# Kernel tuning notes

Hardware: AMD Instinct MI355X
Metric: run time of the kernel (lower is better)

The kernel has to match this reference:

```python
import jax, jax.numpy as jnp
import numpy as np

FORGET_BIAS = 1.0  # TF LSTMCell default

def _lstm_step(c, h, x, W, b):
    # TF BasicLSTM/LSTMCell gate order: i, j (cell candidate), f, o
    z = jnp.concatenate([x, h], axis=-1) @ W + b
    i, j, f, o = jnp.split(z, 4, axis=-1)
    c_new = c * jax.nn.sigmoid(f + FORGET_BIAS) + jax.nn.sigmoid(i) * jnp.tanh(j)
    h_new = jnp.tanh(c_new) * jax.nn.sigmoid(o)
    return c_new, h_new

def setup_inputs() -> dict:
    key = jax.random.key(0)
    k1, k2, k3 = jax.random.split(key, 3)
    B, T, D, H1, H2 = 512, 2048, 1, 64, 1
    x = jax.random.normal(k1, (B, T, D), dtype=jnp.float32)
    W1 = jax.random.normal(k2, (D + H1, 4 * H1), dtype=jnp.float32) * 0.1
    b1 = jnp.zeros((4 * H1,), dtype=jnp.float32)
    W2 = jax.random.normal(k3, (H1 + H2, 4 * H2), dtype=jnp.float32) * 0.1
    b2 = jnp.zeros((4 * H2,), dtype=jnp.float32)
    return {"x": x, "W1": W1, "b1": b1, "W2": W2, "b2": b2}

def reference(x, W1, b1, W2, b2):
    B = x.shape[0]
    H1 = W1.shape[1] // 4
    H2 = W2.shape[1] // 4
    init = (jnp.zeros((B, H1), x.dtype), jnp.zeros((B, H1), x.dtype),
            jnp.zeros((B, H2), x.dtype), jnp.zeros((B, H2), x.dtype))

    def step(carry, x_t):
        c1, h1, c2, h2 = carry
        c1, h1 = _lstm_step(c1, h1, x_t, W1, b1)   # layer 1: LSTMCell(64)
        c2, h2 = _lstm_step(c2, h2, h1, W2, b2)    # layer 2: LSTMCell(1)
        return (c1, h1, c2, h2), h2

    xs = jnp.swapaxes(x, 0, 1)           # [T, B, 1]
    _, ys = jax.lax.scan(step, init, xs)  # ys: [T, B, 1]
    return jnp.swapaxes(ys, 0, 1)         # [B, T, 1]
```

## Files before the change

kernel.cpp:

```cpp
#include <hip/hip_runtime.h>

#define TT 2048
#define NB 256

typedef float v2f __attribute__((ext_vector_type(2)));

__device__ __forceinline__ v2f mk2(float a, float b) { v2f r; r.x = a; r.y = b; return r; }
__device__ __forceinline__ float rcpf(float x) { return __builtin_amdgcn_rcpf(x); }
__device__ __forceinline__ float fsig(float x) { return rcpf(1.0f + __expf(-x)); }
__device__ __forceinline__ float ftanh(float x) {
    return fmaf(2.0f, rcpf(1.0f + __expf(-2.0f * x)), -1.0f);
}

template<int C>
__device__ __forceinline__ float dppmov(float s) {
    return __int_as_float(__builtin_amdgcn_update_dpp(
        __float_as_int(s), __float_as_int(s), C, 0xF, 0xF, false));
}
template<int Q>
__device__ __forceinline__ float qbcast(float x) {
    return __int_as_float(__builtin_amdgcn_update_dpp(
        __float_as_int(x), __float_as_int(x), Q * 0x55, 0xF, 0xF, false));
}

__global__ __launch_bounds__(512)
__attribute__((amdgpu_waves_per_eu(2, 2)))
void lstm1_kernel(const float* __restrict__ x,
                  const float* __restrict__ W1,
                  const float* __restrict__ b1,
                  const float* __restrict__ W2,
                  float* __restrict__ zout)
{
    __shared__ __align__(16) float xall[2][TT + 4];
    __shared__ __align__(16) float h1row[2][64];
    __shared__ __align__(16) float part[2][2][4][4][72];
    __shared__ __align__(16) float zpart[2][32][4][4];

    const int tid  = threadIdx.x;
    const int wave = tid >> 6;
    const int lane = tid & 63;
    const int b    = blockIdx.x;

    for (int i = tid; i < TT; i += 512) {
        xall[0][i] = x[(2 * b) * TT + i];
        xall[1][i] = x[(2 * b + 1) * TT + i];
    }
    if (tid < 8) xall[tid & 1][TT + (tid >> 1)] = 0.0f;

    const int eid = wave >> 2;
    const int wq  = wave & 3;

#define DECLP(G, coff, p) const v2f w##G##p = \
    mk2(W1[(1 + 16*wq + 2*(p)) * 256 + (coff) + lane], \
        W1[(2 + 16*wq + 2*(p)) * 256 + (coff) + lane]);
    DECLP(I,   0, 0) DECLP(I,   0, 1) DECLP(I,   0, 2) DECLP(I,   0, 3)
    DECLP(I,   0, 4) DECLP(I,   0, 5) DECLP(I,   0, 6) DECLP(I,   0, 7)
    DECLP(J,  64, 0) DECLP(J,  64, 1) DECLP(J,  64, 2) DECLP(J,  64, 3)
    DECLP(J,  64, 4) DECLP(J,  64, 5) DECLP(J,  64, 6) DECLP(J,  64, 7)
    DECLP(F, 128, 0) DECLP(F, 128, 1) DECLP(F, 128, 2) DECLP(F, 128, 3)
    DECLP(F, 128, 4) DECLP(F, 128, 5) DECLP(F, 128, 6) DECLP(F, 128, 7)
    DECLP(O, 192, 0) DECLP(O, 192, 1) DECLP(O, 192, 2) DECLP(O, 192, 3)
    DECLP(O, 192, 4) DECLP(O, 192, 5) DECLP(O, 192, 6) DECLP(O, 192, 7)
#undef DECLP

    const int gB   = lane & 3;
    const int uB   = (wq << 4) + (lane >> 2);
    const int colB = (gB << 6) + uB;
    const float w0x   = W1[colB];
    const float biasF = b1[colB] + ((gB == 2) ? 1.0f : 0.0f);
    const float nlm   = (gB == 1) ? -2.0f : -1.0f;
    const bool  isj   = (gB == 1);
    const float w2own = W2[uB * 4 + gB];
    const int   gidx  = (12 + (lane & 3) + ((lane >> 2) << 4)) & 63;

    float c1 = 0.0f;

    if (tid < 128) ((float*)h1row)[tid] = 0.0f;
    __syncthreads();

    float* __restrict__ zb = zout + (size_t)(2 * b + eid) * TT * 4;

    float* __restrict__ pw = &part[eid][0][wq][0][lane];
    const float* __restrict__ pr = &part[eid][0][0][gB][uB];

#define PK4(p, hx, hy)                                                        \
    aI = __builtin_elementwise_fma(mk2(hx, hy), wI##p, aI);                   \
    aJ = __builtin_elementwise_fma(mk2(hx, hy), wJ##p, aJ);                   \
    aF = __builtin_elementwise_fma(mk2(hx, hy), wF##p, aF);                   \
    aO = __builtin_elementwise_fma(mk2(hx, hy), wO##p, aO);

#define STEP(P, t, xv)                                                        \
    {                                                                         \
              \
        if ((t) < TT) {                                                       \
            const float4* hp = (const float4*)&h1row[eid][wq << 4];           \
            const float4 q0 = hp[0], q1 = hp[1], q2 = hp[2], q3 = hp[3];      \
            v2f aI = mk2(0.f, 0.f), aJ = mk2(0.f, 0.f);                       \
            v2f aF = mk2(0.f, 0.f), aO = mk2(0.f, 0.f);                       \
            PK4(0, q0.x, q0.y) PK4(1, q0.z, q0.w)                             \
            PK4(2, q1.x, q1.y) PK4(3, q1.z, q1.w)                             \
            PK4(4, q2.x, q2.y) PK4(5, q2.z, q2.w)                             \
            PK4(6, q3.x, q3.y) PK4(7, q3.z, q3.w)                             \
            pw[(P)*1152 + 0*72] = aI.x + aI.y;                                \
            pw[(P)*1152 + 1*72] = aJ.x + aJ.y;                                \
            pw[(P)*1152 + 2*72] = aF.x + aF.y;                                \
            pw[(P)*1152 + 3*72] = aO.x + aO.y;                                \
        }                                                                     \
        __syncthreads();                       \
          \
        if ((t) >= 16 && (t) <= TT && ((t) & 15) == 0 &&                      \
            wq == (((t) >> 4) & 3)) {                                         \
            const int base = ((t) - 16) & 31;                                 \
            const int s = lane >> 2, gg = lane & 3;                           \
            const float z0 = zpart[eid][base + s][0][gg];                     \
            const float z1 = zpart[eid][base + s][1][gg];                     \
            const float z2 = zpart[eid][base + s][2][gg];                     \
            const float z3 = zpart[eid][base + s][3][gg];                     \
            zb[(size_t)(((t) - 16) + s) * 4 + gg] = (z0 + z1) + (z2 + z3);    \
        }                                                                     \
                       \
        if ((t) < TT) {                                                       \
            const float p0 = pr[(P)*1152 + 0*288];                            \
            const float p1 = pr[(P)*1152 + 1*288];                            \
            const float p2 = pr[(P)*1152 + 2*288];                            \
            const float p3 = pr[(P)*1152 + 3*288];                            \
            const float acc = fmaf((xv), w0x, biasF) + ((p0 + p1)+(p2 + p3)); \
            const float e = __expf(acc * nlm);                                \
            const float r = rcpf(1.0f + e);                                   \
            const float v = isj ? fmaf(2.0f, r, -1.0f) : r;                   \
            const float gi = qbcast<0>(v), gj = qbcast<1>(v);                 \
            const float gf = qbcast<2>(v), go = qbcast<3>(v);                 \
            c1 = fmaf(c1, gf, gi * gj);                                       \
            const float h1v = ftanh(c1) * go;                                 \
            if (gB == 0) h1row[eid][uB] = h1v;      \
                  \
            const float prod = h1v * w2own;                                   \
            float s1 = prod + dppmov<0x114>(prod);             \
            s1 = s1 + dppmov<0x118>(s1);                       \
            const float gv = __shfl(s1, gidx, 64);        \
            float s2 = gv + dppmov<0x114>(gv);                                \
            s2 = s2 + dppmov<0x118>(s2);                                      \
            if ((lane & ~3) == 12)                          \
                zpart[eid][(t) & 31][wq][lane - 12] = s2;                     \
        }                                                                     \
    }

    for (int it = 0; it <= TT; it += 2) {
        const float2 x2 = *(const float2*)&xall[eid][it];
        STEP(0, it,     x2.x)
        STEP(1, it + 1, x2.y)
    }
#undef STEP
#undef PK4
}

__global__ __launch_bounds__(64)
void lstm2_chain(const float* __restrict__ zp,
                 const float* __restrict__ W2,
                 const float* __restrict__ b2,
                 float* __restrict__ out)
{
    const int lane = threadIdx.x & 63;
    const int e    = lane >> 2;
    const int g    = lane & 3;
    const int elem = (blockIdx.x << 4) + e;

    const float w2h = W2[256 + g];
    const float bb  = b2[g] + ((g == 2) ? 1.0f : 0.0f);
    const float nlm = (g == 1) ? -2.0f : -1.0f;
    const float k2  = (g == 1) ?  2.0f :  1.0f;
    const float k3  = (g == 1) ? -1.0f :  0.0f;

    const float* __restrict__ zrow = zp + (size_t)elem * TT * 4 + g;
    float* __restrict__ orow = out + (size_t)elem * TT;

    float c2 = 0.0f, h2 = 0.0f;

    float zc[16];
#pragma unroll
    for (int k = 0; k < 16; ++k) zc[k] = zrow[k << 2];

    for (int t0 = 0; t0 < TT; t0 += 16) {
        float zn[16];
        if (t0 + 16 < TT) {
#pragma unroll
            for (int k = 0; k < 16; ++k) zn[k] = zrow[((t0 + 16 + k) << 2)];
        }
        float st0 = 0.f, st1 = 0.f, st2 = 0.f, st3 = 0.f;
#pragma unroll
        for (int k = 0; k < 16; ++k) {
            const float arg = fmaf(w2h, h2, zc[k] + bb);
            const float ev  = __expf(arg * nlm);
            const float rv  = rcpf(1.0f + ev);
            const float v   = fmaf(k2, rv, k3);
            const float vi = qbcast<0>(v), vj = qbcast<1>(v);
            const float vf = qbcast<2>(v), vo = qbcast<3>(v);
            c2 = fmaf(c2, vf, vi * vj);
            h2 = ftanh(c2) * vo;
            const bool mine = (g == (k & 3));
            if ((k >> 2) == 0) st0 = mine ? h2 : st0;
            else if ((k >> 2) == 1) st1 = mine ? h2 : st1;
            else if ((k >> 2) == 2) st2 = mine ? h2 : st2;
            else st3 = mine ? h2 : st3;
        }
        orow[t0 + g]      = st0;
        orow[t0 + 4 + g]  = st1;
        orow[t0 + 8 + g]  = st2;
        orow[t0 + 12 + g] = st3;
#pragma unroll
        for (int k = 0; k < 16; ++k) zc[k] = zn[k];
    }
}

__global__ __launch_bounds__(512)
__attribute__((amdgpu_waves_per_eu(4, 4)))
void lstm2_mono(const float* __restrict__ x,
                const float* __restrict__ W1,
                const float* __restrict__ b1,
                const float* __restrict__ W2,
                const float* __restrict__ b2,
                float* __restrict__ out)
{
    __shared__ __align__(16) float xall[TT + 4];
    __shared__ __align__(16) float h1x[2][80];
    __shared__ __align__(16) float zpq[4][4];
    __shared__ __align__(16) float h2buf[2][64];

    const int tid  = threadIdx.x;
    const int wave = tid >> 6;
    const int lane = tid & 63;
    const int b    = blockIdx.x;

    for (int i = tid; i < TT; i += 512) xall[i] = x[b * TT + i];
    if (tid < 4) xall[TT + tid] = 0.0f;

    const int u    = lane >> 3;
    const int h    = (lane >> 2) & 1;
    const int g    = lane & 3;
    const int unit = (wave << 3) + u;
    const int col  = (g << 6) + unit;

#define DECLW(k) const v2f wq##k = mk2(W1[(1 + 32*h + 2*(k)) * 256 + col], \
                                       W1[(2 + 32*h + 2*(k)) * 256 + col]);
    DECLW(0)  DECLW(1)  DECLW(2)  DECLW(3)
    DECLW(4)  DECLW(5)  DECLW(6)  DECLW(7)
    DECLW(8)  DECLW(9)  DECLW(10) DECLW(11)
    DECLW(12) DECLW(13) DECLW(14) DECLW(15)
#undef DECLW

    const float w0x   = (h == 0) ? W1[col] : 0.0f;
    const float biasF = (h == 0) ? (b1[col] + ((g == 2) ? 1.0f : 0.0f)) : 0.0f;
    const float nlm   = (g == 1) ? -2.0f : -1.0f;
    const bool  isj   = (g == 1);

    const float w2g  = W2[lane * 4 + (wave & 3)];
    const float w2h0 = W2[256], w2h1 = W2[257], w2h2 = W2[258], w2h3 = W2[259];
    const float b20 = b2[0], b21 = b2[1], b22 = b2[2], b23 = b2[3];

    float c1 = 0.0f;
    float c2 = 0.0f, h2v = 0.0f;

    const int hbase = h * 48;
    const int ridx  = lane + ((lane >> 5) << 4);
    const int widx  = (unit < 32) ? unit : unit + 16;

    if (tid < 160) ((float*)h1x)[tid] = 0.0f;
    __syncthreads();

    float* __restrict__ outb = out + b * TT;

#define WSUM(s) ({ float _s = (s);                                            \
    _s += dppmov<0x111>(_s); _s += dppmov<0x112>(_s); _s += dppmov<0x114>(_s);\
    _s += dppmov<0x118>(_s); _s += dppmov<0x142>(_s); _s += dppmov<0x143>(_s);\
    _s; })

#define STEP(P, t, xv)                                                        \
    {                                                                         \
        if ((t) < TT) {                                                       \
            const float4* hp = (const float4*)&h1x[P][hbase];                 \
            const float4 q0 = hp[0], q1 = hp[1], q2 = hp[2], q3 = hp[3];      \
            const float4 q4 = hp[4], q5 = hp[5], q6 = hp[6], q7 = hp[7];      \
            v2f a0 = mk2(fmaf((xv), w0x, biasF), 0.0f);                       \
            v2f a1 = mk2(0.f, 0.f), a2 = mk2(0.f, 0.f), a3 = mk2(0.f, 0.f);  \
            a0 = __builtin_elementwise_fma(mk2(q0.x, q0.y), wq0,  a0);        \
            a1 = __builtin_elementwise_fma(mk2(q0.z, q0.w), wq1,  a1);        \
            a2 = __builtin_elementwise_fma(mk2(q1.x, q1.y), wq2,  a2);        \
            a3 = __builtin_elementwise_fma(mk2(q1.z, q1.w), wq3,  a3);        \
            a0 = __builtin_elementwise_fma(mk2(q2.x, q2.y), wq4,  a0);        \
            a1 = __builtin_elementwise_fma(mk2(q2.z, q2.w), wq5,  a1);        \
            a2 = __builtin_elementwise_fma(mk2(q3.x, q3.y), wq6,  a2);        \
            a3 = __builtin_elementwise_fma(mk2(q3.z, q3.w), wq7,  a3);        \
            a0 = __builtin_elementwise_fma(mk2(q4.x, q4.y), wq8,  a0);        \
            a1 = __builtin_elementwise_fma(mk2(q4.z, q4.w), wq9,  a1);        \
            a2 = __builtin_elementwise_fma(mk2(q5.x, q5.y), wq10, a2);        \
            a3 = __builtin_elementwise_fma(mk2(q5.z, q5.w), wq11, a3);        \
            a0 = __builtin_elementwise_fma(mk2(q6.x, q6.y), wq12, a0);        \
            a1 = __builtin_elementwise_fma(mk2(q6.z, q6.w), wq13, a1);        \
            a2 = __builtin_elementwise_fma(mk2(q7.x, q7.y), wq14, a2);        \
            a3 = __builtin_elementwise_fma(mk2(q7.z, q7.w), wq15, a3);        \
            const v2f sv = (a0 + a1) + (a2 + a3);                             \
            const float zh = sv.x + sv.y;                                     \
            const float tshr = dppmov<0x114>(zh);                             \
            const float tshl = dppmov<0x104>(zh);                             \
            const float zfull = zh + (h ? tshr : tshl);                       \
            const float e = __expf(zfull * nlm);                              \
            const float r = rcpf(1.0f + e);                                   \
            const float v = isj ? fmaf(2.0f, r, -1.0f) : r;                   \
            const float gi = qbcast<0>(v), gj = qbcast<1>(v);                 \
            const float gf = qbcast<2>(v), go = qbcast<3>(v);                 \
            c1 = fmaf(c1, gf, gi * gj);                                       \
            const float h1v = ftanh(c1) * go;                                 \
            if ((lane & 7) == 0) h1x[(P) ^ 1][widx] = h1v;                    \
        }                                                                     \
        if (wave < 4 && (t) >= 1 && (t) <= TT) {                              \
            const float s = WSUM(h1x[P][ridx] * w2g);                         \
            if (lane == 63) zpq[((t) - 1) & 3][wave] = s;                     \
        }                                                                     \
        if (wave == 7 && lane == 0 && (t) >= 2 && (t) <= TT + 1) {            \
            const int st = (t) - 2;                                           \
            const float4 z4 = *(const float4*)zpq[st & 3];                    \
            const float zi = z4.x + fmaf(h2v, w2h0, b20);                     \
            const float zj = z4.y + fmaf(h2v, w2h1, b21);                     \
            const float zf = z4.z + fmaf(h2v, w2h2, b22);                     \
            const float zo = z4.w + fmaf(h2v, w2h3, b23);                     \
            c2 = c2 * fsig(zf + 1.0f) + fsig(zi) * ftanh(zj);                 \
            h2v = ftanh(c2) * fsig(zo);                                       \
            h2buf[(st >> 6) & 1][st & 63] = h2v;                              \
        }                                                                     \
        __syncthreads();                                                      \
        if (wave == 4 && (t) >= 66 && ((t) & 63) == 2) {                      \
            const int blk = ((t) - 66) >> 6;                                  \
            outb[(blk << 6) + lane] = h2buf[blk & 1][lane];                   \
        }                                                                     \
    }

    for (int it = 0; it <= TT + 2; it += 2) {
        const float2 x2 = *(const float2*)&xall[it];
        STEP(0, it,     x2.x)
        STEP(1, it + 1, x2.y)
    }
#undef STEP
#undef WSUM
}

extern "C" void kernel_launch(void* const* d_in, const int* in_sizes, int n_in,
                              void* d_out, int out_size, void* d_ws, size_t ws_size,
                              hipStream_t stream)
{
    const float* x  = (const float*)d_in[0];
    const float* W1 = (const float*)d_in[1];
    const float* b1 = (const float*)d_in[2];
    const float* W2 = (const float*)d_in[3];
    const float* b2 = (const float*)d_in[4];
    float* out = (float*)d_out;

    const size_t need = (size_t)512 * TT * 4 * sizeof(float);
    if (ws_size >= need) {
        float* zp = (float*)d_ws;
        lstm1_kernel<<<NB, 512, 0, stream>>>(x, W1, b1, W2, zp);
        lstm2_chain<<<512 / 16, 64, 0, stream>>>(zp, W2, b2, out);
    } else {
        lstm2_mono<<<512, 512, 0, stream>>>(x, W1, b1, W2, b2, out);
    }
}
```

Before: 1.231 ms.

## Rewrite layer-1 LSTM as one-wave-per-sequence kernel using fp16 dot2

Replaces the 512-thread, 4-wave-split layer-1 kernel with a single 64-lane wave per batch element. Each lane owns one hidden unit and all four gates, holding W1 in registers as packed fp16 and using fdot2 instructions. This removes the per-step block barrier and the LDS partial-sum reduction. The hidden state goes through a 16-deep fp16 ring in LDS, and the layer-2 input projection is computed in bursts every 16 steps. The risk is reduced precision in the recurrent matmul from fp16 weights and hidden state, plus one lane doing 128 dot2 ops serially per step.

```diff
diff --git a/kernel.cpp b/kernel.cpp
--- a/kernel.cpp
+++ b/kernel.cpp
@@ -1,9 +1,9 @@
 #include <hip/hip_runtime.h>
 
 #define TT 2048
-#define NB 256
 
 typedef float v2f __attribute__((ext_vector_type(2)));
+typedef _Float16 h2v __attribute__((ext_vector_type(2)));
 
 __device__ __forceinline__ v2f mk2(float a, float b) { v2f r; r.x = a; r.y = b; return r; }
 __device__ __forceinline__ float rcpf(float x) { return __builtin_amdgcn_rcpf(x); }
@@ -23,135 +23,122 @@
         __float_as_int(x), __float_as_int(x), Q * 0x55, 0xF, 0xF, false));
 }
 
-__global__ __launch_bounds__(512)
+#if __has_builtin(__builtin_amdgcn_fdot2)
+#define DOT2(a, b, c) __builtin_amdgcn_fdot2((a), (b), (c), false)
+#else
+#define DOT2(a, b, c) fmaf((float)(a).x, (float)(b).x, \
+                      fmaf((float)(a).y, (float)(b).y, (c)))
+#endif
+
+__device__ __forceinline__ h2v pk2(float a, float b) {
+#if __has_builtin(__builtin_amdgcn_cvt_pkrtz)
+    return __builtin_bit_cast(h2v, __builtin_amdgcn_cvt_pkrtz(a, b));
+#else
+    h2v r; r.x = (_Float16)a; r.y = (_Float16)b; return r;
+#endif
+}
+__device__ __forceinline__ h2v bch(int v) { return __builtin_bit_cast(h2v, v); }
+
+__global__ __launch_bounds__(64)
 __attribute__((amdgpu_waves_per_eu(2, 2)))
-void lstm1_kernel(const float* __restrict__ x,
-                  const float* __restrict__ W1,
-                  const float* __restrict__ b1,
-                  const float* __restrict__ W2,
-                  float* __restrict__ zout)
+void lstm1_f16(const float* __restrict__ x,
+               const float* __restrict__ W1,
+               const float* __restrict__ b1,
+               const float* __restrict__ W2,
+               float* __restrict__ zout)
 {
-    __shared__ __align__(16) float xall[2][TT + 4];
-    __shared__ __align__(16) float h1row[2][64];
-    __shared__ __align__(16) float part[2][2][4][4][72];
-    __shared__ __align__(16) float zpart[2][32][4][4];
-
-    const int tid  = threadIdx.x;
-    const int wave = tid >> 6;
-    const int lane = tid & 63;
-    const int b    = blockIdx.x;
-
-    for (int i = tid; i < TT; i += 512) {
-        xall[0][i] = x[(2 * b) * TT + i];
-        xall[1][i] = x[(2 * b + 1) * TT + i];
-    }
-    if (tid < 8) xall[tid & 1][TT + (tid >> 1)] = 0.0f;
-
-    const int eid = wave >> 2;
-    const int wq  = wave & 3;
-
-#define DECLP(G, coff, p) const v2f w##G##p = \
-    mk2(W1[(1 + 16*wq + 2*(p)) * 256 + (coff) + lane], \
-        W1[(2 + 16*wq + 2*(p)) * 256 + (coff) + lane]);
-    DECLP(I,   0, 0) DECLP(I,   0, 1) DECLP(I,   0, 2) DECLP(I,   0, 3)
-    DECLP(I,   0, 4) DECLP(I,   0, 5) DECLP(I,   0, 6) DECLP(I,   0, 7)
-    DECLP(J,  64, 0) DECLP(J,  64, 1) DECLP(J,  64, 2) DECLP(J,  64, 3)
-    DECLP(J,  64, 4) DECLP(J,  64, 5) DECLP(J,  64, 6) DECLP(J,  64, 7)
-    DECLP(F, 128, 0) DECLP(F, 128, 1) DECLP(F, 128, 2) DECLP(F, 128, 3)
-    DECLP(F, 128, 4) DECLP(F, 128, 5) DECLP(F, 128, 6) DECLP(F, 128, 7)
-    DECLP(O, 192, 0) DECLP(O, 192, 1) DECLP(O, 192, 2) DECLP(O, 192, 3)
-    DECLP(O, 192, 4) DECLP(O, 192, 5) DECLP(O, 192, 6) DECLP(O, 192, 7)
-#undef DECLP
-
-    const int gB   = lane & 3;
-    const int uB   = (wq << 4) + (lane >> 2);
-    const int colB = (gB << 6) + uB;
-    const float w0x   = W1[colB];
-    const float biasF = b1[colB] + ((gB == 2) ? 1.0f : 0.0f);
-    const float nlm   = (gB == 1) ? -2.0f : -1.0f;
-    const bool  isj   = (gB == 1);
-    const float w2own = W2[uB * 4 + gB];
-    const int   gidx  = (12 + (lane & 3) + ((lane >> 2) << 4)) & 63;
+    __shared__ __align__(16) float xall[TT];
+    __shared__ __align__(16) _Float16 hring[16 * 72];
+
+    const int lane = threadIdx.x & 63;
+    const int e    = blockIdx.x;
+    const int u    = lane;
+
+    for (int i = lane; i < TT; i += 64) xall[i] = x[(size_t)e * TT + i];
+    for (int i = lane; i < 576; i += 64) ((int*)hring)[i] = 0;
+
+#define DWQ(G, GO, q) \
+    const h2v w##G##q##x = pk2(W1[(1+8*(q))*256 + (GO)*64 + u], W1[(2+8*(q))*256 + (GO)*64 + u]); \
+    const h2v w##G##q##y = pk2(W1[(3+8*(q))*256 + (GO)*64 + u], W1[(4+8*(q))*256 + (GO)*64 + u]); \
+    const h2v w##G##q##z = pk2(W1[(5+8*(q))*256 + (GO)*64 + u], W1[(6+8*(q))*256 + (GO)*64 + u]); \
+    const h2v w##G##q##w = pk2(W1[(7+8*(q))*256 + (GO)*64 + u], W1[(8+8*(q))*256 + (GO)*64 + u]);
+    DWQ(I, 0, 0) DWQ(I, 0, 1) DWQ(I, 0, 2) DWQ(I, 0, 3)
+    DWQ(I, 0, 4) DWQ(I, 0, 5) DWQ(I, 0, 6) DWQ(I, 0, 7)
+    DWQ(J, 1, 0) DWQ(J, 1, 1) DWQ(J, 1, 2) DWQ(J, 1, 3)
+    DWQ(J, 1, 4) DWQ(J, 1, 5) DWQ(J, 1, 6) DWQ(J, 1, 7)
+    DWQ(F, 2, 0) DWQ(F, 2, 1) DWQ(F, 2, 2) DWQ(F, 2, 3)
+    DWQ(F, 2, 4) DWQ(F, 2, 5) DWQ(F, 2, 6) DWQ(F, 2, 7)
+    DWQ(O, 3, 0) DWQ(O, 3, 1) DWQ(O, 3, 2) DWQ(O, 3, 3)
+    DWQ(O, 3, 4) DWQ(O, 3, 5) DWQ(O, 3, 6) DWQ(O, 3, 7)
+#undef DWQ
+
+    const float w0I = W1[u],        bI = b1[u];
+    const float w0J = W1[64 + u],   bJ = b1[64 + u];
+    const float w0F = W1[128 + u],  bF = b1[128 + u] + 1.0f;
+    const float w0O = W1[192 + u],  bO = b1[192 + u];
+
+    const int tl = lane >> 2, gq = lane & 3;
+#define DW2(q) \
+    const h2v w2##q##x = pk2(W2[(8*(q)+0)*4 + gq], W2[(8*(q)+1)*4 + gq]); \
+    const h2v w2##q##y = pk2(W2[(8*(q)+2)*4 + gq], W2[(8*(q)+3)*4 + gq]); \
+    const h2v w2##q##z = pk2(W2[(8*(q)+4)*4 + gq], W2[(8*(q)+5)*4 + gq]); \
+    const h2v w2##q##w = pk2(W2[(8*(q)+6)*4 + gq], W2[(8*(q)+7)*4 + gq]);
+    DW2(0) DW2(1) DW2(2) DW2(3) DW2(4) DW2(5) DW2(6) DW2(7)
+#undef DW2
 
     float c1 = 0.0f;
-
-    if (tid < 128) ((float*)h1row)[tid] = 0.0f;
     __syncthreads();
 
-    float* __restrict__ zb = zout + (size_t)(2 * b + eid) * TT * 4;
-
-    float* __restrict__ pw = &part[eid][0][wq][0][lane];
-    const float* __restrict__ pr = &part[eid][0][0][gB][uB];
-
-#define PK4(p, hx, hy)                                                        \
-    aI = __builtin_elementwise_fma(mk2(hx, hy), wI##p, aI);                   \
-    aJ = __builtin_elementwise_fma(mk2(hx, hy), wJ##p, aJ);                   \
-    aF = __builtin_elementwise_fma(mk2(hx, hy), wF##p, aF);                   \
-    aO = __builtin_elementwise_fma(mk2(hx, hy), wO##p, aO);
-
-#define STEP(P, t, xv)                                                        \
-    {                                                                         \
-              \
-        if ((t) < TT) {                                                       \
-            const float4* hp = (const float4*)&h1row[eid][wq << 4];           \
-            const float4 q0 = hp[0], q1 = hp[1], q2 = hp[2], q3 = hp[3];      \
-            v2f aI = mk2(0.f, 0.f), aJ = mk2(0.f, 0.f);                       \
-            v2f aF = mk2(0.f, 0.f), aO = mk2(0.f, 0.f);                       \
-            PK4(0, q0.x, q0.y) PK4(1, q0.z, q0.w)                             \
-            PK4(2, q1.x, q1.y) PK4(3, q1.z, q1.w)                             \
-            PK4(4, q2.x, q2.y) PK4(5, q2.z, q2.w)                             \
-            PK4(6, q3.x, q3.y) PK4(7, q3.z, q3.w)                             \
-            pw[(P)*1152 + 0*72] = aI.x + aI.y;                                \
-            pw[(P)*1152 + 1*72] = aJ.x + aJ.y;                                \
-            pw[(P)*1152 + 2*72] = aF.x + aF.y;                                \
-            pw[(P)*1152 + 3*72] = aO.x + aO.y;                                \
-        }                                                                     \
-        __syncthreads();                       \
-          \
-        if ((t) >= 16 && (t) <= TT && ((t) & 15) == 0 &&                      \
-            wq == (((t) >> 4) & 3)) {                                         \
-            const int base = ((t) - 16) & 31;                                 \
-            const int s = lane >> 2, gg = lane & 3;                           \
-            const float z0 = zpart[eid][base + s][0][gg];                     \
-            const float z1 = zpart[eid][base + s][1][gg];                     \
-            const float z2 = zpart[eid][base + s][2][gg];                     \
-            const float z3 = zpart[eid][base + s][3][gg];                     \
-            zb[(size_t)(((t) - 16) + s) * 4 + gg] = (z0 + z1) + (z2 + z3);    \
-        }                                                                     \
-                       \
-        if ((t) < TT) {                                                       \
-            const float p0 = pr[(P)*1152 + 0*288];                            \
-            const float p1 = pr[(P)*1152 + 1*288];                            \
-            const float p2 = pr[(P)*1152 + 2*288];                            \
-            const float p3 = pr[(P)*1152 + 3*288];                            \
-            const float acc = fmaf((xv), w0x, biasF) + ((p0 + p1)+(p2 + p3)); \
-            const float e = __expf(acc * nlm);                                \
-            const float r = rcpf(1.0f + e);                                   \
-            const float v = isj ? fmaf(2.0f, r, -1.0f) : r;                   \
-            const float gi = qbcast<0>(v), gj = qbcast<1>(v);                 \
-            const float gf = qbcast<2>(v), go = qbcast<3>(v);                 \
-            c1 = fmaf(c1, gf, gi * gj);                                       \
-            const float h1v = ftanh(c1) * go;                                 \
-            if (gB == 0) h1row[eid][uB] = h1v;      \
-                  \
-            const float prod = h1v * w2own;                                   \
-            float s1 = prod + dppmov<0x114>(prod);             \
-            s1 = s1 + dppmov<0x118>(s1);                       \
-            const float gv = __shfl(s1, gidx, 64);        \
-            float s2 = gv + dppmov<0x114>(gv);                                \
-            s2 = s2 + dppmov<0x118>(s2);                                      \
-            if ((lane & ~3) == 12)                          \
-                zpart[eid][(t) & 31][wq][lane - 12] = s2;                     \
-        }                                                                     \
-    }
-
-    for (int it = 0; it <= TT; it += 2) {
-        const float2 x2 = *(const float2*)&xall[eid][it];
-        STEP(0, it,     x2.x)
-        STEP(1, it + 1, x2.y)
-    }
-#undef STEP
-#undef PK4
+    float* __restrict__ zb = zout + (size_t)e * TT * 4;
+
+#define DGQ(G, q, v) \
+    acc##G = DOT2(bch((v).x), w##G##q##x, acc##G); \
+    acc##G = DOT2(bch((v).y), w##G##q##y, acc##G); \
+    acc##G = DOT2(bch((v).z), w##G##q##z, acc##G); \
+    acc##G = DOT2(bch((v).w), w##G##q##w, acc##G);
+
+    for (int t = 0; t < TT; ++t) {
+        const int4* hp = (const int4*)&hring[((t - 1) & 15) * 72];
+        const int4 q0 = hp[0], q1 = hp[1], q2 = hp[2], q3 = hp[3];
+        const int4 q4 = hp[4], q5 = hp[5], q6 = hp[6], q7 = hp[7];
+        const float xt = xall[t];
+        float accI = fmaf(xt, w0I, bI);
+        float accJ = fmaf(xt, w0J, bJ);
+        float accF = fmaf(xt, w0F, bF);
+        float accO = fmaf(xt, w0O, bO);
+        DGQ(I, 0, q0) DGQ(J, 0, q0) DGQ(F, 0, q0) DGQ(O, 0, q0)
+        DGQ(I, 1, q1) DGQ(J, 1, q1) DGQ(F, 1, q1) DGQ(O, 1, q1)
+        DGQ(I, 2, q2) DGQ(J, 2, q2) DGQ(F, 2, q2) DGQ(O, 2, q2)
+        DGQ(I, 3, q3) DGQ(J, 3, q3) DGQ(F, 3, q3) DGQ(O, 3, q3)
+        DGQ(I, 4, q4) DGQ(J, 4, q4) DGQ(F, 4, q4) DGQ(O, 4, q4)
+        DGQ(I, 5, q5) DGQ(J, 5, q5) DGQ(F, 5, q5) DGQ(O, 5, q5)
+        DGQ(I, 6, q6) DGQ(J, 6, q6) DGQ(F, 6, q6) DGQ(O, 6, q6)
+        DGQ(I, 7, q7) DGQ(J, 7, q7) DGQ(F, 7, q7) DGQ(O, 7, q7)
+        const float i_ = fsig(accI);
+        const float j_ = ftanh(accJ);
+        const float f_ = fsig(accF);
+        const float o_ = fsig(accO);
+        c1 = fmaf(c1, f_, i_ * j_);
+        const float h1 = ftanh(c1) * o_;
+        hring[(t & 15) * 72 + u] = (_Float16)h1;
+
+        if ((t & 15) == 15) {
+            const int4* hb = (const int4*)&hring[tl * 72];
+            const int4 b0 = hb[0], b1q = hb[1], b2q = hb[2], b3 = hb[3];
+            const int4 b4 = hb[4], b5 = hb[5], b6 = hb[6], b7 = hb[7];
+            float z2 = 0.0f;
+#define BQ(q, v) \
+            z2 = DOT2(bch((v).x), w2##q##x, z2); \
+            z2 = DOT2(bch((v).y), w2##q##y, z2); \
+            z2 = DOT2(bch((v).z), w2##q##z, z2); \
+            z2 = DOT2(bch((v).w), w2##q##w, z2);
+            BQ(0, b0) BQ(1, b1q) BQ(2, b2q) BQ(3, b3)
+            BQ(4, b4) BQ(5, b5) BQ(6, b6) BQ(7, b7)
+#undef BQ
+            zb[(size_t)(t - 15 + tl) * 4 + gq] = z2;
+        }
+    }
+#undef DGQ
 }
 
 __global__ __launch_bounds__(64)
@@ -258,7 +245,7 @@
     const float b20 = b2[0], b21 = b2[1], b22 = b2[2], b23 = b2[3];
 
     float c1 = 0.0f;
-    float c2 = 0.0f, h2v = 0.0f;
+    float c2 = 0.0f, h2v2 = 0.0f;
 
     const int hbase = h * 48;
     const int ridx  = lane + ((lane >> 5) << 4);
@@ -319,13 +306,13 @@
         if (wave == 7 && lane == 0 && (t) >= 2 && (t) <= TT + 1) {            \
             const int st = (t) - 2;                                           \
             const float4 z4 = *(const float4*)zpq[st & 3];                    \
-            const float zi = z4.x + fmaf(h2v, w2h0, b20);                     \
-            const float zj = z4.y + fmaf(h2v, w2h1, b21);                     \
-            const float zf = z4.z + fmaf(h2v, w2h2, b22);                     \
-            const float zo = z4.w + fmaf(h2v, w2h3, b23);                     \
+            const float zi = z4.x + fmaf(h2v2, w2h0, b20);                    \
+            const float zj = z4.y + fmaf(h2v2, w2h1, b21);                    \
+            const float zf = z4.z + fmaf(h2v2, w2h2, b22);                    \
+            const float zo = z4.w + fmaf(h2v2, w2h3, b23);                    \
             c2 = c2 * fsig(zf + 1.0f) + fsig(zi) * ftanh(zj);                 \
-            h2v = ftanh(c2) * fsig(zo);                                       \
-            h2buf[(st >> 6) & 1][st & 63] = h2v;                              \
+            h2v2 = ftanh(c2) * fsig(zo);                                      \
+            h2buf[(st >> 6) & 1][st & 63] = h2v2;                             \
         }                                                                     \
         __syncthreads();                                                      \
         if (wave == 4 && (t) >= 66 && ((t) & 63) == 2) {                      \
@@ -357,7 +344,7 @@
     const size_t need = (size_t)512 * TT * 4 * sizeof(float);
     if (ws_size >= need) {
         float* zp = (float*)d_ws;
-        lstm1_kernel<<<NB, 512, 0, stream>>>(x, W1, b1, W2, zp);
+        lstm1_f16<<<512, 64, 0, stream>>>(x, W1, b1, W2, zp);
         lstm2_chain<<<512 / 16, 64, 0, stream>>>(zp, W2, b2, out);
     } else {
         lstm2_mono<<<512, 512, 0, stream>>>(x, W1, b1, W2, b2, out);
```

After: 1.039 ms. 1.18x faster.
